# Performance work log

Hardware: AMD Instinct MI355X
Metric: run time of the kernel (lower is better)

## Reference

```python
import jax, jax.numpy as jnp
import numpy as np

B, IN, OUT = 1024, 512, 64000
EPS = 1e-12  # matches torch F.normalize eps


def setup_inputs() -> dict:
    key = jax.random.key(0)
    k1, k2, k3 = jax.random.split(key, 3)
    x = jax.random.normal(k1, (B, IN), dtype=jnp.float32)
    label = jax.random.randint(k2, (B,), 0, OUT)
    # xavier_uniform_ for weight [OUT, IN]: limit = sqrt(6 / (fan_in + fan_out))
    limit = float(np.sqrt(6.0 / (IN + OUT)))
    weight = jax.random.uniform(k3, (OUT, IN), dtype=jnp.float32, minval=-limit, maxval=limit)
    s = 50               # python scalar; set via _calculate_para but UNUSED in normfree output
    m = jnp.full((1,), 0.5, dtype=jnp.float32)  # margin
    return {"x": x, "label": label, "weight": weight, "s": s, "m": m}


def reference(x, label, weight, s, m):
    m = m.reshape(())
    cos_m, sin_m = jnp.cos(m), jnp.sin(m)
    # norm of raw input (the 'normfree' scale replacing s)
    norm = jnp.linalg.norm(x, axis=1, keepdims=True)            # [B, 1]
    xn = x / jnp.maximum(norm, EPS)                             # F.normalize(input)
    wn = weight / jnp.maximum(
        jnp.linalg.norm(weight, axis=1, keepdims=True), EPS)    # F.normalize(weight)
    cosine = xn @ wn.T                                          # [B, OUT]
    sine = jnp.sqrt(jnp.clip(1.0 - cosine * cosine, 0.0, None))
    phi = cosine * cos_m - sine * sin_m                         # cos(theta + m)
    # per-sample loop in torch == one-hot substitution only where cosine > 0
    onehot = jax.nn.one_hot(label, OUT, dtype=bool)             # [B, OUT]
    mod_cosine = jnp.where(onehot & (cosine > 0), phi, cosine)
    return norm * mod_cosine, wn
```

## Files before the change

kernel.cpp:

```cpp
#include <hip/hip_runtime.h>
#include <cstdint>

#define EPSN 1e-12f
static constexpr int B_ROWS = 1024;
static constexpr int IN_DIM = 512;
static constexpr int OUT_DIM = 64000;

typedef __attribute__((ext_vector_type(8))) short bf16x8;
typedef __attribute__((ext_vector_type(4))) float f32x4;

__device__ __forceinline__ unsigned short f2bf(float f) {
  uint32_t u = __builtin_bit_cast(uint32_t, f);
  u += 0x7fffu + ((u >> 16) & 1u);
  return (unsigned short)(u >> 16);
}

__device__ __forceinline__ float bf2f(unsigned short h) {
  uint32_t u = (uint32_t)h << 16;
  return __builtin_bit_cast(float, u);
}

__device__ __forceinline__ float wave_sum(float v) {
#pragma unroll
  for (int off = 32; off; off >>= 1) v += __shfl_xor(v, off);
  return v;
}

__device__ __forceinline__ void async16(const void* g, void* l) {
  __builtin_amdgcn_global_load_lds((const __attribute__((address_space(1))) uint32_t*)g,
                                   (__attribute__((address_space(3))) uint32_t*)l, 16, 0, 0);
}

__global__ void prep_kernel(const float* __restrict__ X, const int* __restrict__ label,
                            const float* __restrict__ Wg, float* __restrict__ norms,
                            float* __restrict__ fixdot, unsigned short* __restrict__ xbf) {
  int lane = threadIdx.x & 63;
  int row = blockIdx.x * 4 + (threadIdx.x >> 6);
  const float* src = X + (size_t)row * IN_DIM + lane * 8;
  float4 a = *(const float4*)src;
  float4 b = *(const float4*)(src + 4);
  uint4 u;
  u.x = (uint32_t)f2bf(a.x) | ((uint32_t)f2bf(a.y) << 16);
  u.y = (uint32_t)f2bf(a.z) | ((uint32_t)f2bf(a.w) << 16);
  u.z = (uint32_t)f2bf(b.x) | ((uint32_t)f2bf(b.y) << 16);
  u.w = (uint32_t)f2bf(b.z) | ((uint32_t)f2bf(b.w) << 16);
  *(uint4*)(xbf + (size_t)row * IN_DIM + lane * 8) = u;
  float ssx = a.x * a.x;
  ssx = fmaf(a.y, a.y, ssx); ssx = fmaf(a.z, a.z, ssx); ssx = fmaf(a.w, a.w, ssx);
  ssx = fmaf(b.x, b.x, ssx); ssx = fmaf(b.y, b.y, ssx); ssx = fmaf(b.z, b.z, ssx);
  ssx = fmaf(b.w, b.w, ssx);
  int lab = label[row];
  const float* wsrc = Wg + (size_t)lab * IN_DIM + lane * 8;
  float4 wa = *(const float4*)wsrc, wb = *(const float4*)(wsrc + 4);
  float d = a.x * wa.x;
  d = fmaf(a.y, wa.y, d); d = fmaf(a.z, wa.z, d); d = fmaf(a.w, wa.w, d);
  d = fmaf(b.x, wb.x, d); d = fmaf(b.y, wb.y, d); d = fmaf(b.z, wb.z, d);
  d = fmaf(b.w, wb.w, d);
  float ssw = wa.x * wa.x;
  ssw = fmaf(wa.y, wa.y, ssw); ssw = fmaf(wa.z, wa.z, ssw); ssw = fmaf(wa.w, wa.w, ssw);
  ssw = fmaf(wb.x, wb.x, ssw); ssw = fmaf(wb.y, wb.y, ssw); ssw = fmaf(wb.z, wb.z, ssw);
  ssw = fmaf(wb.w, wb.w, ssw);
  ssx = wave_sum(ssx);
  d = wave_sum(d);
  ssw = wave_sum(ssw);
  if (lane == 0) {
    norms[row] = sqrtf(ssx);
    fixdot[row] = d / fmaxf(sqrtf(ssw), EPSN);
  }
}

__global__ void wcast_kernel(const float* __restrict__ Wg, unsigned short* __restrict__ wbf) {
  int lane = threadIdx.x & 63;
  int row = blockIdx.x * 4 + (threadIdx.x >> 6);
  const float* src = Wg + (size_t)row * IN_DIM + lane * 8;
  float4 a = *(const float4*)src;
  float4 b = *(const float4*)(src + 4);
  float ss = a.x * a.x;
  ss = fmaf(a.y, a.y, ss); ss = fmaf(a.z, a.z, ss); ss = fmaf(a.w, a.w, ss);
  ss = fmaf(b.x, b.x, ss); ss = fmaf(b.y, b.y, ss); ss = fmaf(b.z, b.z, ss);
  ss = fmaf(b.w, b.w, ss);
  ss = wave_sum(ss);
  float inv = 1.0f / fmaxf(sqrtf(ss), EPSN);
  uint4 u;
  u.x = (uint32_t)f2bf(a.x * inv) | ((uint32_t)f2bf(a.y * inv) << 16);
  u.y = (uint32_t)f2bf(a.z * inv) | ((uint32_t)f2bf(a.w * inv) << 16);
  u.z = (uint32_t)f2bf(b.x * inv) | ((uint32_t)f2bf(b.y * inv) << 16);
  u.w = (uint32_t)f2bf(b.z * inv) | ((uint32_t)f2bf(b.w * inv) << 16);
  *(uint4*)(wbf + (size_t)row * IN_DIM + lane * 8) = u;
}

__global__ __launch_bounds__(256, 2) void gemm_epi_kernel(
    const unsigned short* __restrict__ Abf, const unsigned short* __restrict__ Bbf,
    const float* __restrict__ norms, const float* __restrict__ fixdot,
    const int* __restrict__ label, const float* __restrict__ mArr,
    float* __restrict__ out0, float* __restrict__ wnOut) {
  __shared__ char smem[73728];

  const int t = threadIdx.x;
  int flat = blockIdx.x;
  int xcd = flat & 7;
  int wk = (flat >> 3) + xcd * 250;
  int mT = wk & 3, nT = wk >> 2;
  int rowA0 = mT * 256, rowB0 = nT * 128;

  int lane = t & 63;
  int wid = t >> 6;
  int wm = wid >> 1, wn2 = wid & 1;
  int rl = lane & 15, sl = lane >> 4;

  const unsigned short* aP[4];
  const unsigned short* bP[2];
#pragma unroll
  for (int c = 0; c < 4; ++c) {
    int ch = t + c * 256;
    int r = ch >> 2, q = (ch & 3) ^ ((r >> 1) & 3);
    aP[c] = Abf + (size_t)(rowA0 + r) * IN_DIM + q * 8;
  }
#pragma unroll
  for (int c = 0; c < 2; ++c) {
    int ch = t + c * 256;
    int r = ch >> 2, q = (ch & 3) ^ ((r >> 1) & 3);
    bP[c] = Bbf + (size_t)(rowB0 + r) * IN_DIM + q * 8;
  }

  auto issueSub = [&](int sig, int slot) {
    int kcol = sig * 32;
    char* aD = smem + slot * 24576;
    char* bD = aD + 16384;
#pragma unroll
    for (int c = 0; c < 4; ++c) async16(aP[c] + kcol, aD + (t + c * 256) * 16);
#pragma unroll
    for (int c = 0; c < 2; ++c) async16(bP[c] + kcol, bD + (t + c * 256) * 16);
  };

  issueSub(0, 0); issueSub(1, 1);

  f32x4 acc[8][4];
#pragma unroll
  for (int m = 0; m < 8; ++m)
#pragma unroll
    for (int n = 0; n < 4; ++n) acc[m][n] = (f32x4){0.f, 0.f, 0.f, 0.f};

  int slotR = 0, slotW = 2;
#pragma unroll 1
  for (int sigma = 0; sigma < 16; ++sigma) {
    __builtin_amdgcn_sched_barrier(0);
    if (sigma <= 14) asm volatile("s_waitcnt vmcnt(6)" ::: "memory");
    else             asm volatile("s_waitcnt vmcnt(0)" ::: "memory");
    __builtin_amdgcn_s_barrier();
    __builtin_amdgcn_sched_barrier(0);
    if (sigma <= 13) issueSub(sigma + 2, slotW);

    const char* aB = smem + slotR * 24576;
    const char* bB = aB + 16384;
    bf16x8 av[8], bv[4];
#pragma unroll
    for (int m = 0; m < 8; ++m) {
      int r = wm * 128 + m * 16 + rl;
      av[m] = *(const bf16x8*)(aB + r * 64 + ((sl ^ ((r >> 1) & 3)) * 16));
    }
#pragma unroll
    for (int n = 0; n < 4; ++n) {
      int r = wn2 * 64 + n * 16 + rl;
      bv[n] = *(const bf16x8*)(bB + r * 64 + ((sl ^ ((r >> 1) & 3)) * 16));
    }
    __builtin_amdgcn_s_setprio(1);
#pragma unroll
    for (int n = 0; n < 4; ++n)
#pragma unroll
      for (int m = 0; m < 8; ++m)
        acc[m][n] = __builtin_amdgcn_mfma_f32_16x16x32_bf16(av[m], bv[n], acc[m][n], 0, 0, 0);
    __builtin_amdgcn_s_setprio(0);
    slotR = (slotR == 2) ? 0 : slotR + 1;
    slotW = (slotW == 2) ? 0 : slotW + 1;
  }

  {
    int r = t >> 3;
    int c0 = (t & 7) * 64;
    int row = rowB0 + mT * 32 + r;
    const unsigned short* srcp = Bbf + (size_t)row * IN_DIM + c0;
    float* dst = wnOut + (size_t)row * IN_DIM + c0;
#pragma unroll
    for (int g = 0; g < 8; ++g) {
      uint4 uu = *(const uint4*)(srcp + g * 8);
      float4 f;
      f.x = bf2f((unsigned short)(uu.x & 0xffff)); f.y = bf2f((unsigned short)(uu.x >> 16));
      f.z = bf2f((unsigned short)(uu.y & 0xffff)); f.w = bf2f((unsigned short)(uu.y >> 16));
      *(float4*)(dst + g * 8) = f;
      f.x = bf2f((unsigned short)(uu.z & 0xffff)); f.y = bf2f((unsigned short)(uu.z >> 16));
      f.z = bf2f((unsigned short)(uu.w & 0xffff)); f.w = bf2f((unsigned short)(uu.w >> 16));
      *(float4*)(dst + g * 8 + 4) = f;
    }
  }

  float mm = mArr[0];
  float cm = cosf(mm), sm = sinf(mm);
  int rowb = rowA0 + wm * 128, colb = rowB0 + wn2 * 64;
#pragma unroll
  for (int m = 0; m < 8; ++m) {
#pragma unroll
    for (int q = 0; q < 4; ++q) {
      int R = rowb + m * 16 + sl * 4 + q;
      int lab = label[R];
      float nv = norms[R], fv = fixdot[R];
      float* orow = out0 + (size_t)R * OUT_DIM;
#pragma unroll
      for (int n = 0; n < 4; ++n) {
        int Cc = colb + n * 16 + rl;
        float val = acc[m][n][q];
        if (Cc == lab) {
          float c = fv / fmaxf(nv, EPSN);
          val = (c > 0.f) ? nv * (c * cm - sqrtf(fmaxf(1.f - c * c, 0.f)) * sm) : fv;
        }
        orow[Cc] = val;
      }
    }
  }
}

extern "C" void kernel_launch(void* const* d_in, const int* in_sizes, int n_in,
                              void* d_out, int out_size, void* d_ws, size_t ws_size,
                              hipStream_t stream) {
  const float* x = (const float*)d_in[0];
  const int* label = (const int*)d_in[1];
  const float* weight = (const float*)d_in[2];
  const float* mArr = (const float*)d_in[4];

  float* out0 = (float*)d_out;
  float* wnOut = out0 + (size_t)B_ROWS * OUT_DIM;

  char* ws = (char*)d_ws;
  float* norms = (float*)ws;
  float* fixdot = (float*)(ws + 4096);
  unsigned short* xbf = (unsigned short*)(ws + 8192);
  unsigned short* wbf = (unsigned short*)(ws + 8192 + 2ull * B_ROWS * IN_DIM);

  prep_kernel<<<B_ROWS / 4, 256, 0, stream>>>(x, label, weight, norms, fixdot, xbf);
  wcast_kernel<<<OUT_DIM / 4, 256, 0, stream>>>(weight, wbf);
  gemm_epi_kernel<<<2000, 256, 0, stream>>>(xbf, wbf, norms, fixdot, label, mArr,
                                            out0, wnOut);
}
```

Baseline: 214.2 us.

## Fuse weight normalization and bf16 cast into GEMM B-operand loading

Drops the separate wcast kernel and its bf16 weight workspace. Each GEMM block now computes the inverse norms of its 128 weight rows into LDS and writes its share of the fp32 normalized weight output directly. The B operand is loaded as fp32 into registers, scaled and converted to bf16, then stored into a double-buffered LDS tile, while A stays on async global-to-LDS loads. This removes a full write and re-read of the bf16 weight copy and one launch. In exchange each of the four M-tile blocks re-reads the fp32 weight rows, twice the bytes of bf16, and the synchronous register staging adds latency and register pressure inside the pipelined loop.

```diff
diff --git a/kernel.cpp b/kernel.cpp
--- a/kernel.cpp
+++ b/kernel.cpp
@@ -13,11 +13,6 @@
   uint32_t u = __builtin_bit_cast(uint32_t, f);
   u += 0x7fffu + ((u >> 16) & 1u);
   return (unsigned short)(u >> 16);
-}
-
-__device__ __forceinline__ float bf2f(unsigned short h) {
-  uint32_t u = (uint32_t)h << 16;
-  return __builtin_bit_cast(float, u);
 }
 
 __device__ __forceinline__ float wave_sum(float v) {
@@ -69,32 +64,13 @@
   }
 }
 
-__global__ void wcast_kernel(const float* __restrict__ Wg, unsigned short* __restrict__ wbf) {
-  int lane = threadIdx.x & 63;
-  int row = blockIdx.x * 4 + (threadIdx.x >> 6);
-  const float* src = Wg + (size_t)row * IN_DIM + lane * 8;
-  float4 a = *(const float4*)src;
-  float4 b = *(const float4*)(src + 4);
-  float ss = a.x * a.x;
-  ss = fmaf(a.y, a.y, ss); ss = fmaf(a.z, a.z, ss); ss = fmaf(a.w, a.w, ss);
-  ss = fmaf(b.x, b.x, ss); ss = fmaf(b.y, b.y, ss); ss = fmaf(b.z, b.z, ss);
-  ss = fmaf(b.w, b.w, ss);
-  ss = wave_sum(ss);
-  float inv = 1.0f / fmaxf(sqrtf(ss), EPSN);
-  uint4 u;
-  u.x = (uint32_t)f2bf(a.x * inv) | ((uint32_t)f2bf(a.y * inv) << 16);
-  u.y = (uint32_t)f2bf(a.z * inv) | ((uint32_t)f2bf(a.w * inv) << 16);
-  u.z = (uint32_t)f2bf(b.x * inv) | ((uint32_t)f2bf(b.y * inv) << 16);
-  u.w = (uint32_t)f2bf(b.z * inv) | ((uint32_t)f2bf(b.w * inv) << 16);
-  *(uint4*)(wbf + (size_t)row * IN_DIM + lane * 8) = u;
-}
-
-__global__ __launch_bounds__(256, 2) void gemm_epi_kernel(
-    const unsigned short* __restrict__ Abf, const unsigned short* __restrict__ Bbf,
+__global__ __launch_bounds__(256, 2) void gemm_fused_kernel(
+    const float* __restrict__ Wg, const unsigned short* __restrict__ Abf,
     const float* __restrict__ norms, const float* __restrict__ fixdot,
     const int* __restrict__ label, const float* __restrict__ mArr,
     float* __restrict__ out0, float* __restrict__ wnOut) {
-  __shared__ char smem[73728];
+  __shared__ char smem[66048];
+  float* invnL = (float*)(smem + 65536);
 
   const int t = threadIdx.x;
   int flat = blockIdx.x;
@@ -108,32 +84,95 @@
   int wm = wid >> 1, wn2 = wid & 1;
   int rl = lane & 15, sl = lane >> 4;
 
+#pragma unroll 1
+  for (int pass = 0; pass < 2; ++pass) {
+    int r = pass * 64 + (t >> 2);
+    const float* src = Wg + (size_t)(rowB0 + r) * IN_DIM + (t & 3) * 128;
+    float s = 0.f;
+#pragma unroll
+    for (int j = 0; j < 32; ++j) {
+      float4 v = ((const float4*)src)[j];
+      s = fmaf(v.x, v.x, s); s = fmaf(v.y, v.y, s);
+      s = fmaf(v.z, v.z, s); s = fmaf(v.w, v.w, s);
+    }
+    s += __shfl_xor(s, 1);
+    s += __shfl_xor(s, 2);
+    if ((t & 3) == 0) invnL[r] = 1.0f / fmaxf(sqrtf(s), EPSN);
+  }
+  __syncthreads();
+
+  {
+    int r = mT * 32 + (t >> 3);
+    float inv = invnL[r];
+    const float* src = Wg + (size_t)(rowB0 + r) * IN_DIM + (t & 7) * 64;
+    float* dst = wnOut + (size_t)(rowB0 + r) * IN_DIM + (t & 7) * 64;
+#pragma unroll
+    for (int j = 0; j < 16; ++j) {
+      float4 v = ((const float4*)src)[j];
+      v.x *= inv; v.y *= inv; v.z *= inv; v.w *= inv;
+      ((float4*)dst)[j] = v;
+    }
+  }
+
+  int rB0i = t >> 2, qB0i = t & 3;
+  int rB1i = rB0i + 64;
+  float invB0 = invnL[rB0i], invB1 = invnL[rB1i];
+  const float* bW0 = Wg + (size_t)(rowB0 + rB0i) * IN_DIM + qB0i * 8;
+  const float* bW1 = Wg + (size_t)(rowB0 + rB1i) * IN_DIM + qB0i * 8;
+  int bOff0 = rB0i * 64 + ((qB0i ^ ((rB0i >> 1) & 3)) * 16);
+  int bOff1 = rB1i * 64 + ((qB0i ^ ((rB1i >> 1) & 3)) * 16);
+
   const unsigned short* aP[4];
-  const unsigned short* bP[2];
 #pragma unroll
   for (int c = 0; c < 4; ++c) {
     int ch = t + c * 256;
     int r = ch >> 2, q = (ch & 3) ^ ((r >> 1) & 3);
     aP[c] = Abf + (size_t)(rowA0 + r) * IN_DIM + q * 8;
   }
-#pragma unroll
-  for (int c = 0; c < 2; ++c) {
-    int ch = t + c * 256;
-    int r = ch >> 2, q = (ch & 3) ^ ((r >> 1) & 3);
-    bP[c] = Bbf + (size_t)(rowB0 + r) * IN_DIM + q * 8;
-  }
-
-  auto issueSub = [&](int sig, int slot) {
+
+  auto issueA = [&](int sig) {
+    char* aD = smem + 16384 + (sig % 3) * 16384;
     int kcol = sig * 32;
-    char* aD = smem + slot * 24576;
-    char* bD = aD + 16384;
 #pragma unroll
     for (int c = 0; c < 4; ++c) async16(aP[c] + kcol, aD + (t + c * 256) * 16);
-#pragma unroll
-    for (int c = 0; c < 2; ++c) async16(bP[c] + kcol, bD + (t + c * 256) * 16);
   };
 
-  issueSub(0, 0); issueSub(1, 1);
+  float4 hB[4];
+  auto loadB = [&](int sig) {
+    int kcol = sig * 32;
+    hB[0] = *(const float4*)(bW0 + kcol);
+    hB[1] = *(const float4*)(bW0 + kcol + 4);
+    hB[2] = *(const float4*)(bW1 + kcol);
+    hB[3] = *(const float4*)(bW1 + kcol + 4);
+  };
+  auto writeB = [&](int sig, const float4* h) {
+    char* bD = smem + (sig & 1) * 8192;
+    uint4 u;
+    u.x = (uint32_t)f2bf(h[0].x * invB0) | ((uint32_t)f2bf(h[0].y * invB0) << 16);
+    u.y = (uint32_t)f2bf(h[0].z * invB0) | ((uint32_t)f2bf(h[0].w * invB0) << 16);
+    u.z = (uint32_t)f2bf(h[1].x * invB0) | ((uint32_t)f2bf(h[1].y * invB0) << 16);
+    u.w = (uint32_t)f2bf(h[1].z * invB0) | ((uint32_t)f2bf(h[1].w * invB0) << 16);
+    *(uint4*)(bD + bOff0) = u;
+    u.x = (uint32_t)f2bf(h[2].x * invB1) | ((uint32_t)f2bf(h[2].y * invB1) << 16);
+    u.y = (uint32_t)f2bf(h[2].z * invB1) | ((uint32_t)f2bf(h[2].w * invB1) << 16);
+    u.z = (uint32_t)f2bf(h[3].x * invB1) | ((uint32_t)f2bf(h[3].y * invB1) << 16);
+    u.w = (uint32_t)f2bf(h[3].z * invB1) | ((uint32_t)f2bf(h[3].w * invB1) << 16);
+    *(uint4*)(bD + bOff1) = u;
+  };
+
+  asm volatile("s_waitcnt vmcnt(0)" ::: "memory");
+  float4 hB0[4];
+  {
+    hB0[0] = *(const float4*)(bW0);
+    hB0[1] = *(const float4*)(bW0 + 4);
+    hB0[2] = *(const float4*)(bW1);
+    hB0[3] = *(const float4*)(bW1 + 4);
+  }
+  issueA(0);
+  loadB(1);
+  issueA(1);
+  asm volatile("s_waitcnt vmcnt(12)" ::: "memory");
+  writeB(0, hB0);
 
   f32x4 acc[8][4];
 #pragma unroll
@@ -141,18 +180,19 @@
 #pragma unroll
     for (int n = 0; n < 4; ++n) acc[m][n] = (f32x4){0.f, 0.f, 0.f, 0.f};
 
-  int slotR = 0, slotW = 2;
 #pragma unroll 1
   for (int sigma = 0; sigma < 16; ++sigma) {
     __builtin_amdgcn_sched_barrier(0);
-    if (sigma <= 14) asm volatile("s_waitcnt vmcnt(6)" ::: "memory");
-    else             asm volatile("s_waitcnt vmcnt(0)" ::: "memory");
+    if (sigma <= 14) asm volatile("s_waitcnt vmcnt(4) lgkmcnt(0)" ::: "memory");
+    else             asm volatile("s_waitcnt vmcnt(0) lgkmcnt(0)" ::: "memory");
     __builtin_amdgcn_s_barrier();
     __builtin_amdgcn_sched_barrier(0);
-    if (sigma <= 13) issueSub(sigma + 2, slotW);
-
-    const char* aB = smem + slotR * 24576;
-    const char* bB = aB + 16384;
+
+    if (sigma + 1 <= 15) writeB(sigma + 1, hB);
+    if (sigma + 2 <= 15) { loadB(sigma + 2); issueA(sigma + 2); }
+
+    const char* aB = smem + 16384 + (sigma % 3) * 16384;
+    const char* bB = smem + (sigma & 1) * 8192;
     bf16x8 av[8], bv[4];
 #pragma unroll
     for (int m = 0; m < 8; ++m) {
@@ -171,27 +211,6 @@
       for (int m = 0; m < 8; ++m)
         acc[m][n] = __builtin_amdgcn_mfma_f32_16x16x32_bf16(av[m], bv[n], acc[m][n], 0, 0, 0);
     __builtin_amdgcn_s_setprio(0);
-    slotR = (slotR == 2) ? 0 : slotR + 1;
-    slotW = (slotW == 2) ? 0 : slotW + 1;
-  }
-
-  {
-    int r = t >> 3;
-    int c0 = (t & 7) * 64;
-    int row = rowB0 + mT * 32 + r;
-    const unsigned short* srcp = Bbf + (size_t)row * IN_DIM + c0;
-    float* dst = wnOut + (size_t)row * IN_DIM + c0;
-#pragma unroll
-    for (int g = 0; g < 8; ++g) {
-      uint4 uu = *(const uint4*)(srcp + g * 8);
-      float4 f;
-      f.x = bf2f((unsigned short)(uu.x & 0xffff)); f.y = bf2f((unsigned short)(uu.x >> 16));
-      f.z = bf2f((unsigned short)(uu.y & 0xffff)); f.w = bf2f((unsigned short)(uu.y >> 16));
-      *(float4*)(dst + g * 8) = f;
-      f.x = bf2f((unsigned short)(uu.z & 0xffff)); f.y = bf2f((unsigned short)(uu.z >> 16));
-      f.z = bf2f((unsigned short)(uu.w & 0xffff)); f.w = bf2f((unsigned short)(uu.w >> 16));
-      *(float4*)(dst + g * 8 + 4) = f;
-    }
   }
 
   float mm = mArr[0];
@@ -234,10 +253,8 @@
   float* norms = (float*)ws;
   float* fixdot = (float*)(ws + 4096);
   unsigned short* xbf = (unsigned short*)(ws + 8192);
-  unsigned short* wbf = (unsigned short*)(ws + 8192 + 2ull * B_ROWS * IN_DIM);
 
   prep_kernel<<<B_ROWS / 4, 256, 0, stream>>>(x, label, weight, norms, fixdot, xbf);
-  wcast_kernel<<<OUT_DIM / 4, 256, 0, stream>>>(weight, wbf);
-  gemm_epi_kernel<<<2000, 256, 0, stream>>>(xbf, wbf, norms, fixdot, label, mArr,
-                                            out0, wnOut);
-}
+  gemm_fused_kernel<<<2000, 256, 0, stream>>>(weight, xbf, norms, fixdot, label,
+                                              mArr, out0, wnOut);
+}
```

After: 244.6 us. 1.14x slower.
